# Kernel tuning notes

Hardware: AMD Instinct MI355X
Metric: run time of the kernel (lower is better)

The kernel has to match this reference:

```python
import jax, jax.numpy as jnp
import numpy as np

NOISE_STD = 0.1

def setup_inputs() -> dict:
    key = jax.random.key(0)
    k1, k2, k3, k4 = jax.random.split(key, 4)
    B, S, D, E, NS = 4, 4096, 2048, 64, 10
    x = jax.random.normal(k1, (B, S, D), dtype=jnp.float32)
    W = jax.random.normal(k2, (E, D), dtype=jnp.float32) * (1.0 / np.sqrt(D))
    scale_condition = jax.random.normal(k3, (NS, 1, 1), dtype=jnp.float32)
    noise = jax.random.normal(k4, (B, S, E), dtype=jnp.float32)
    return {"x": x, "W": W, "scale_condition": scale_condition, "noise": noise, "scale_idx": 3}

def reference(x, W, scale_condition, noise, scale_idx):
    TOP_K = 2
    E = W.shape[0]
    # scale modulation: scale_condition[scale_idx] has shape [1,1], broadcasts over [B,S,D]
    scale_factor = scale_condition[scale_idx]
    router_input = x * (1.0 + scale_factor * 0.1)
    # small GEMM: [B,S,D] x [D,E] -> [B,S,E]
    router_logits = jnp.einsum('bsd,ed->bse', router_input, W)
    router_logits = router_logits + noise * NOISE_STD
    routing_probs = jax.nn.softmax(router_logits, axis=-1)
    routing_weights, selected_experts = jax.lax.top_k(routing_probs, TOP_K)
    routing_weights = routing_weights / jnp.sum(routing_weights, axis=-1, keepdims=True)
    # scatter top-k normalized weights into dense [B,S,E] dispatch tensor
    dispatch_tensor = jnp.sum(
        jax.nn.one_hot(selected_experts, E, dtype=routing_weights.dtype)
        * routing_weights[..., None],
        axis=-2,
    )
    return dispatch_tensor, routing_probs, selected_experts
```

## Files before the change

kernel.cpp:

```cpp
#include <hip/hip_runtime.h>
#include <math.h>

#define D        2048
#define E        64
#define NROWS    16384
#define BM       32
#define BK       64
#define NT       256
#define KITERS   (D / BK)

__global__ __launch_bounds__(NT)
void gemm_kernel(const float* __restrict__ x,
                 const float* __restrict__ W,
                 const float* __restrict__ scond,
                 const float* __restrict__ noise,
                 const int* __restrict__ sidx,
                 float* __restrict__ logits_out)
{
    __shared__ float4 xs[BM][17];
    __shared__ float4 ws[BK][16];

    const int tid = threadIdx.x;
    const int rowBase = blockIdx.x * BM;

    const float factor = 1.0f + 0.1f * scond[sidx[0]];

    const int xk = tid & 15;
    const int xr = tid >> 4;
    const int we = tid & 63;
    const int wk = tid >> 6;

    const int eg = tid & 15;
    const int rg = tid >> 4;
    const int e0 = eg << 2;

    float acc[2][4];
#pragma unroll
    for (int i = 0; i < 2; ++i)
#pragma unroll
        for (int j = 0; j < 4; ++j) acc[i][j] = 0.f;

    const float* xg = x + (size_t)rowBase * D;

    float4 xb[2], wb[4];
#pragma unroll
    for (int i = 0; i < 2; ++i)
        xb[i] = *(const float4*)(xg + (xr + 16 * i) * D + (xk << 2));
#pragma unroll
    for (int j = 0; j < 4; ++j)
        wb[j] = *(const float4*)(W + we * D + (wk << 4) + (j << 2));

    for (int t = 0; t < KITERS; ++t) {
#pragma unroll
        for (int i = 0; i < 2; ++i) {
            float4 v = xb[i];
            v.x *= factor; v.y *= factor; v.z *= factor; v.w *= factor;
            xs[xr + 16 * i][xk] = v;
        }
        {
            float* wsf = (float*)ws;
#pragma unroll
            for (int j = 0; j < 4; ++j) {
                const int kk = (wk << 4) + (j << 2);
                wsf[(kk + 0) * E + we] = wb[j].x;
                wsf[(kk + 1) * E + we] = wb[j].y;
                wsf[(kk + 2) * E + we] = wb[j].z;
                wsf[(kk + 3) * E + we] = wb[j].w;
            }
        }
        __syncthreads();

        if (t + 1 < KITERS) {
            const int k0 = (t + 1) * BK;
#pragma unroll
            for (int i = 0; i < 2; ++i)
                xb[i] = *(const float4*)(xg + (xr + 16 * i) * D + k0 + (xk << 2));
#pragma unroll
            for (int j = 0; j < 4; ++j)
                wb[j] = *(const float4*)(W + we * D + k0 + (wk << 4) + (j << 2));
        }

#pragma unroll
        for (int kg = 0; kg < 16; ++kg) {
            float4 xv[2], wv[4];
#pragma unroll
            for (int i = 0; i < 2; ++i) xv[i] = xs[rg + 16 * i][kg];
#pragma unroll
            for (int c = 0; c < 4; ++c) wv[c] = ws[(kg << 2) + c][eg];
#pragma unroll
            for (int i = 0; i < 2; ++i) {
                const float x0 = xv[i].x, x1 = xv[i].y, x2 = xv[i].z, x3 = xv[i].w;
                acc[i][0] += x0 * wv[0].x; acc[i][1] += x0 * wv[0].y;
                acc[i][2] += x0 * wv[0].z; acc[i][3] += x0 * wv[0].w;
                acc[i][0] += x1 * wv[1].x; acc[i][1] += x1 * wv[1].y;
                acc[i][2] += x1 * wv[1].z; acc[i][3] += x1 * wv[1].w;
                acc[i][0] += x2 * wv[2].x; acc[i][1] += x2 * wv[2].y;
                acc[i][2] += x2 * wv[2].z; acc[i][3] += x2 * wv[2].w;
                acc[i][0] += x3 * wv[3].x; acc[i][1] += x3 * wv[3].y;
                acc[i][2] += x3 * wv[3].z; acc[i][3] += x3 * wv[3].w;
            }
        }
        __syncthreads();
    }

#pragma unroll
    for (int i = 0; i < 2; ++i) {
        const int gRow = rowBase + rg + 16 * i;
        const float4 nz = *(const float4*)(noise + (size_t)gRow * E + e0);
        float4 o;
        o.x = acc[i][0] + 0.1f * nz.x;
        o.y = acc[i][1] + 0.1f * nz.y;
        o.z = acc[i][2] + 0.1f * nz.z;
        o.w = acc[i][3] + 0.1f * nz.w;
        *(float4*)(logits_out + (size_t)gRow * E + e0) = o;
    }
}

__global__ __launch_bounds__(256)
void topk_kernel(float* __restrict__ probs,
                 float* __restrict__ dispatch,
                 float* __restrict__ sel)
{
    const int lane = threadIdx.x & 63;
    const int wave = threadIdx.x >> 6;
    const int row  = blockIdx.x * 4 + wave;

    const float v = probs[(size_t)row * E + lane];

    float m = v;
#pragma unroll
    for (int off = 32; off > 0; off >>= 1)
        m = fmaxf(m, __shfl_xor(m, off, 64));
    const float p = expf(v - m);
    float s = p;
#pragma unroll
    for (int off = 32; off > 0; off >>= 1)
        s += __shfl_xor(s, off, 64);
    const float prob = p / s;
    probs[(size_t)row * E + lane] = prob;

    float bv = prob; int bi = lane;
#pragma unroll
    for (int off = 32; off > 0; off >>= 1) {
        const float ov = __shfl_xor(bv, off, 64);
        const int   oi = __shfl_xor(bi, off, 64);
        if (ov > bv || (ov == bv && oi < bi)) { bv = ov; bi = oi; }
    }
    float cv = (lane == bi) ? -INFINITY : prob;
    int ci = lane;
#pragma unroll
    for (int off = 32; off > 0; off >>= 1) {
        const float ov = __shfl_xor(cv, off, 64);
        const int   oi = __shfl_xor(ci, off, 64);
        if (ov > cv || (ov == cv && oi < ci)) { cv = ov; ci = oi; }
    }

    const float sum2 = bv + cv;
    float dval = 0.f;
    if (lane == bi) dval = bv / sum2;
    if (lane == ci) dval = cv / sum2;
    dispatch[(size_t)row * E + lane] = dval;

    if (lane == 0) {
        float2 sv; sv.x = (float)bi; sv.y = (float)ci;
        *(float2*)(sel + (size_t)row * 2) = sv;
    }
}

extern "C" void kernel_launch(void* const* d_in, const int* in_sizes, int n_in,
                              void* d_out, int out_size, void* d_ws, size_t ws_size,
                              hipStream_t stream) {
    const float* x     = (const float*)d_in[0];
    const float* W     = (const float*)d_in[1];
    const float* scond = (const float*)d_in[2];
    const float* noise = (const float*)d_in[3];
    const int*   sidx  = (const int*)d_in[4];

    float* out      = (float*)d_out;
    float* dispatch = out;
    float* probs    = out + (size_t)NROWS * E;
    float* sel      = out + 2 * (size_t)NROWS * E;

    gemm_kernel<<<dim3(NROWS / BM), dim3(NT), 0, stream>>>(
        x, W, scond, noise, sidx, probs);
    topk_kernel<<<dim3(NROWS / 4), dim3(256), 0, stream>>>(
        probs, dispatch, sel);
}
```

Before: 246.1 us.

## Stream x tiles into LDS via direct global-to-LDS loads, read W as uniform loads

```diff
diff --git a/kernel.cpp b/kernel.cpp
--- a/kernel.cpp
+++ b/kernel.cpp
@@ -4,12 +4,11 @@
 #define D        2048
 #define E        64
 #define NROWS    16384
-#define BM       32
 #define BK       64
-#define NT       256
 #define KITERS   (D / BK)
+#define XSTRIDE  68
 
-__global__ __launch_bounds__(NT)
+__global__ __launch_bounds__(512)
 void gemm_kernel(const float* __restrict__ x,
                  const float* __restrict__ W,
                  const float* __restrict__ scond,
@@ -17,103 +16,82 @@
                  const int* __restrict__ sidx,
                  float* __restrict__ logits_out)
 {
-    __shared__ float4 xs[BM][17];
-    __shared__ float4 ws[BK][16];
+    __shared__ float xs[2][64 * XSTRIDE];
 
-    const int tid = threadIdx.x;
-    const int rowBase = blockIdx.x * BM;
+    const int tid  = threadIdx.x;
+    const int lane = tid & 63;
+    const int wv   = tid >> 6;
+    const int rowBase = blockIdx.x * 64;
+
+    const int e0 = __builtin_amdgcn_readfirstlane(wv << 3);
 
     const float factor = 1.0f + 0.1f * scond[sidx[0]];
 
-    const int xk = tid & 15;
-    const int xr = tid >> 4;
-    const int we = tid & 63;
-    const int wk = tid >> 6;
+    float acc[8];
+#pragma unroll
+    for (int j = 0; j < 8; ++j) acc[j] = 0.f;
 
-    const int eg = tid & 15;
-    const int rg = tid >> 4;
-    const int e0 = eg << 2;
-
-    float acc[2][4];
 #pragma unroll
-    for (int i = 0; i < 2; ++i)
-#pragma unroll
-        for (int j = 0; j < 4; ++j) acc[i][j] = 0.f;
-
-    const float* xg = x + (size_t)rowBase * D;
-
-    float4 xb[2], wb[4];
-#pragma unroll
-    for (int i = 0; i < 2; ++i)
-        xb[i] = *(const float4*)(xg + (xr + 16 * i) * D + (xk << 2));
-#pragma unroll
-    for (int j = 0; j < 4; ++j)
-        wb[j] = *(const float4*)(W + we * D + (wk << 4) + (j << 2));
+    for (int rr = 0; rr < 8; ++rr) {
+        const int r = (wv << 3) + rr;
+        const float* src = x + (size_t)(rowBase + r) * D + lane;
+        __builtin_amdgcn_global_load_lds(
+            (const __attribute__((address_space(1))) void*)src,
+            (__attribute__((address_space(3))) void*)&xs[0][r * XSTRIDE],
+            4, 0, 0);
+    }
+    __syncthreads();
 
     for (int t = 0; t < KITERS; ++t) {
+        const int cur = t & 1;
+
+        if (t + 1 < KITERS) {
+            const int nxt = cur ^ 1;
+            const int kOff = (t + 1) * BK;
 #pragma unroll
-        for (int i = 0; i < 2; ++i) {
-            float4 v = xb[i];
-            v.x *= factor; v.y *= factor; v.z *= factor; v.w *= factor;
-            xs[xr + 16 * i][xk] = v;
-        }
-        {
-            float* wsf = (float*)ws;
-#pragma unroll
-            for (int j = 0; j < 4; ++j) {
-                const int kk = (wk << 4) + (j << 2);
-                wsf[(kk + 0) * E + we] = wb[j].x;
-                wsf[(kk + 1) * E + we] = wb[j].y;
-                wsf[(kk + 2) * E + we] = wb[j].z;
-                wsf[(kk + 3) * E + we] = wb[j].w;
+            for (int rr = 0; rr < 8; ++rr) {
+                const int r = (wv << 3) + rr;
+                const float* src = x + (size_t)(rowBase + r) * D + kOff + lane;
+                __builtin_amdgcn_global_load_lds(
+                    (const __attribute__((address_space(1))) void*)src,
+                    (__attribute__((address_space(3))) void*)&xs[nxt][r * XSTRIDE],
+                    4, 0, 0);
             }
         }
-        __syncthreads();
 
-        if (t + 1 < KITERS) {
-            const int k0 = (t + 1) * BK;
-#pragma unroll
-            for (int i = 0; i < 2; ++i)
-                xb[i] = *(const float4*)(xg + (xr + 16 * i) * D + k0 + (xk << 2));
-#pragma unroll
-            for (int j = 0; j < 4; ++j)
-                wb[j] = *(const float4*)(W + we * D + k0 + (wk << 4) + (j << 2));
-        }
-
+        const float4* xrow = (const float4*)&xs[cur][lane * XSTRIDE];
+        const float*  wbaseT = W + (size_t)e0 * D + t * BK;
 #pragma unroll
         for (int kg = 0; kg < 16; ++kg) {
-            float4 xv[2], wv[4];
+            float4 xv = xrow[kg];
+            xv.x *= factor; xv.y *= factor; xv.z *= factor; xv.w *= factor;
+            const float* wb = wbaseT + (kg << 2);
 #pragma unroll
-            for (int i = 0; i < 2; ++i) xv[i] = xs[rg + 16 * i][kg];
-#pragma unroll
-            for (int c = 0; c < 4; ++c) wv[c] = ws[(kg << 2) + c][eg];
-#pragma unroll
-            for (int i = 0; i < 2; ++i) {
-                const float x0 = xv[i].x, x1 = xv[i].y, x2 = xv[i].z, x3 = xv[i].w;
-                acc[i][0] += x0 * wv[0].x; acc[i][1] += x0 * wv[0].y;
-                acc[i][2] += x0 * wv[0].z; acc[i][3] += x0 * wv[0].w;
-                acc[i][0] += x1 * wv[1].x; acc[i][1] += x1 * wv[1].y;
-                acc[i][2] += x1 * wv[1].z; acc[i][3] += x1 * wv[1].w;
-                acc[i][0] += x2 * wv[2].x; acc[i][1] += x2 * wv[2].y;
-                acc[i][2] += x2 * wv[2].z; acc[i][3] += x2 * wv[2].w;
-                acc[i][0] += x3 * wv[3].x; acc[i][1] += x3 * wv[3].y;
-                acc[i][2] += x3 * wv[3].z; acc[i][3] += x3 * wv[3].w;
+            for (int j = 0; j < 8; ++j) {
+                const float4 wq = *(const float4*)(wb + (size_t)j * D);
+                acc[j] += xv.x * wq.x;
+                acc[j] += xv.y * wq.y;
+                acc[j] += xv.z * wq.z;
+                acc[j] += xv.w * wq.w;
             }
         }
         __syncthreads();
     }
 
-#pragma unroll
-    for (int i = 0; i < 2; ++i) {
-        const int gRow = rowBase + rg + 16 * i;
-        const float4 nz = *(const float4*)(noise + (size_t)gRow * E + e0);
-        float4 o;
-        o.x = acc[i][0] + 0.1f * nz.x;
-        o.y = acc[i][1] + 0.1f * nz.y;
-        o.z = acc[i][2] + 0.1f * nz.z;
-        o.w = acc[i][3] + 0.1f * nz.w;
-        *(float4*)(logits_out + (size_t)gRow * E + e0) = o;
-    }
+    const int gRow = rowBase + lane;
+    const float4 n0 = *(const float4*)(noise + (size_t)gRow * E + e0);
+    const float4 n1 = *(const float4*)(noise + (size_t)gRow * E + e0 + 4);
+    float4 o0, o1;
+    o0.x = acc[0] + 0.1f * n0.x;
+    o0.y = acc[1] + 0.1f * n0.y;
+    o0.z = acc[2] + 0.1f * n0.z;
+    o0.w = acc[3] + 0.1f * n0.w;
+    o1.x = acc[4] + 0.1f * n1.x;
+    o1.y = acc[5] + 0.1f * n1.y;
+    o1.z = acc[6] + 0.1f * n1.z;
+    o1.w = acc[7] + 0.1f * n1.w;
+    *(float4*)(logits_out + (size_t)gRow * E + e0)     = o0;
+    *(float4*)(logits_out + (size_t)gRow * E + e0 + 4) = o1;
 }
 
 __global__ __launch_bounds__(256)
@@ -181,7 +159,7 @@
     float* probs    = out + (size_t)NROWS * E;
     float* sel      = out + 2 * (size_t)NROWS * E;
 
-    gemm_kernel<<<dim3(NROWS / BM), dim3(NT), 0, stream>>>(
+    gemm_kernel<<<dim3(NROWS / 64), dim3(512), 0, stream>>>(
         x, W, scond, noise, sidx, probs);
     topk_kernel<<<dim3(NROWS / 4), dim3(256), 0, stream>>>(
         probs, dispatch, sel);
```

After: 444.5 us. 1.81x slower.

## Split-K router GEMM with larger register tiles and fused reduce-softmax-topk

Applied to the files above, without the earlier changes.

```diff
diff --git a/kernel.cpp b/kernel.cpp
--- a/kernel.cpp
+++ b/kernel.cpp
@@ -4,44 +4,193 @@
 #define D        2048
 #define E        64
 #define NROWS    16384
-#define BM       32
-#define BK       64
-#define NT       256
-#define KITERS   (D / BK)
-
-__global__ __launch_bounds__(NT)
-void gemm_kernel(const float* __restrict__ x,
+#define NSLICE   8
+#define KSLICE   (D / NSLICE)
+#define BK       32
+#define TILES    (KSLICE / BK)
+#define BM       128
+#define PARTIAL_BYTES ((size_t)NSLICE * NROWS * E * 4)
+
+__global__ __launch_bounds__(128, 2)
+void gemm_ksplit(const float* __restrict__ x,
                  const float* __restrict__ W,
                  const float* __restrict__ scond,
+                 const int* __restrict__ sidx,
+                 float* __restrict__ partial)
+{
+    __shared__ float4 xsT[8 * 129];
+    __shared__ float  ws [BK * E];
+
+    const int tid   = threadIdx.x;
+    const int slice = blockIdx.x & 7;
+    const int rowBase = (blockIdx.x >> 3) * BM;
+    const int kBase   = slice * KSLICE;
+
+    const float factor = 1.0f + 0.1f * scond[sidx[0]];
+
+    const int sxr = tid >> 3;
+    const int sxc = tid & 7;
+    const int swe = tid & 63;
+    const int swh = tid >> 6;
+
+    const int rg = tid & 15;
+    const int eg = tid >> 4;
+
+    float acc[8][8];
+#pragma unroll
+    for (int i = 0; i < 8; ++i)
+#pragma unroll
+        for (int j = 0; j < 8; ++j) acc[i][j] = 0.f;
+
+    const float* xg = x + (size_t)rowBase * D + kBase;
+    const float* wg = W + (size_t)swe * D + kBase + swh * 16;
+
+    float4 xb[8], wb[4];
+#pragma unroll
+    for (int i = 0; i < 8; ++i)
+        xb[i] = *(const float4*)(xg + (size_t)(sxr + 16 * i) * D + (sxc << 2));
+#pragma unroll
+    for (int j = 0; j < 4; ++j)
+        wb[j] = *(const float4*)(wg + (j << 2));
+
+    for (int t = 0; t < TILES; ++t) {
+#pragma unroll
+        for (int i = 0; i < 8; ++i) {
+            float4 v = xb[i];
+            v.x *= factor; v.y *= factor; v.z *= factor; v.w *= factor;
+            xsT[sxc * 129 + sxr + 16 * i] = v;
+        }
+#pragma unroll
+        for (int j = 0; j < 4; ++j) {
+            const int kk = swh * 16 + (j << 2);
+            ws[(kk + 0) * E + swe] = wb[j].x;
+            ws[(kk + 1) * E + swe] = wb[j].y;
+            ws[(kk + 2) * E + swe] = wb[j].z;
+            ws[(kk + 3) * E + swe] = wb[j].w;
+        }
+        __syncthreads();
+
+        if (t + 1 < TILES) {
+            const int k0 = (t + 1) * BK;
+#pragma unroll
+            for (int i = 0; i < 8; ++i)
+                xb[i] = *(const float4*)(xg + (size_t)(sxr + 16 * i) * D + k0 + (sxc << 2));
+#pragma unroll
+            for (int j = 0; j < 4; ++j)
+                wb[j] = *(const float4*)(wg + k0 + (j << 2));
+        }
+
+        const float4* ws4 = (const float4*)ws;
+#pragma unroll
+        for (int kg = 0; kg < 8; ++kg) {
+            float4 xv[8];
+#pragma unroll
+            for (int i = 0; i < 8; ++i)
+                xv[i] = xsT[kg * 129 + rg + 16 * i];
+#pragma unroll
+            for (int k = 0; k < 4; ++k) {
+                const float4 wa = ws4[((kg << 2) + k) * 16 + (eg << 1)];
+                const float4 wbq = ws4[((kg << 2) + k) * 16 + (eg << 1) + 1];
+#pragma unroll
+                for (int i = 0; i < 8; ++i) {
+                    const float xk = ((const float*)&xv[i])[k];
+                    acc[i][0] += xk * wa.x;  acc[i][1] += xk * wa.y;
+                    acc[i][2] += xk * wa.z;  acc[i][3] += xk * wa.w;
+                    acc[i][4] += xk * wbq.x; acc[i][5] += xk * wbq.y;
+                    acc[i][6] += xk * wbq.z; acc[i][7] += xk * wbq.w;
+                }
+            }
+        }
+        __syncthreads();
+    }
+
+    float* pbase = partial + (size_t)slice * NROWS * E;
+#pragma unroll
+    for (int i = 0; i < 8; ++i) {
+        const int row = rowBase + rg + 16 * i;
+        float4 a0, a1;
+        a0.x = acc[i][0]; a0.y = acc[i][1]; a0.z = acc[i][2]; a0.w = acc[i][3];
+        a1.x = acc[i][4]; a1.y = acc[i][5]; a1.z = acc[i][6]; a1.w = acc[i][7];
+        *(float4*)(pbase + (size_t)row * E + (eg << 3))     = a0;
+        *(float4*)(pbase + (size_t)row * E + (eg << 3) + 4) = a1;
+    }
+}
+
+__global__ __launch_bounds__(256)
+void reduce_topk(const float* __restrict__ partial,
                  const float* __restrict__ noise,
-                 const int* __restrict__ sidx,
-                 float* __restrict__ logits_out)
+                 float* __restrict__ dispatch,
+                 float* __restrict__ probs,
+                 float* __restrict__ sel)
 {
-    __shared__ float4 xs[BM][17];
-    __shared__ float4 ws[BK][16];
-
+    const int lane = threadIdx.x & 63;
+    const int wave = threadIdx.x >> 6;
+    const int row  = blockIdx.x * 4 + wave;
+
+    float v = 0.f;
+#pragma unroll
+    for (int s = 0; s < NSLICE; ++s)
+        v += partial[(size_t)s * NROWS * E + (size_t)row * E + lane];
+    v += 0.1f * noise[(size_t)row * E + lane];
+
+    float m = v;
+#pragma unroll
+    for (int off = 32; off > 0; off >>= 1)
+        m = fmaxf(m, __shfl_xor(m, off, 64));
+    const float p = expf(v - m);
+    float s = p;
+#pragma unroll
+    for (int off = 32; off > 0; off >>= 1)
+        s += __shfl_xor(s, off, 64);
+    const float prob = p / s;
+    probs[(size_t)row * E + lane] = prob;
+
+    float bv = prob; int bi = lane;
+#pragma unroll
+    for (int off = 32; off > 0; off >>= 1) {
+        const float ov = __shfl_xor(bv, off, 64);
+        const int   oi = __shfl_xor(bi, off, 64);
+        if (ov > bv || (ov == bv && oi < bi)) { bv = ov; bi = oi; }
+    }
+    float cv = (lane == bi) ? -INFINITY : prob;
+    int ci = lane;
+#pragma unroll
+    for (int off = 32; off > 0; off >>= 1) {
+        const float ov = __shfl_xor(cv, off, 64);
+        const int   oi = __shfl_xor(ci, off, 64);
+        if (ov > cv || (ov == cv && oi < ci)) { cv = ov; ci = oi; }
+    }
+
+    const float sum2 = bv + cv;
+    float dval = 0.f;
+    if (lane == bi) dval = bv / sum2;
+    if (lane == ci) dval = cv / sum2;
+    dispatch[(size_t)row * E + lane] = dval;
+
+    if (lane == 0) {
+        float2 sv; sv.x = (float)bi; sv.y = (float)ci;
+        *(float2*)(sel + (size_t)row * 2) = sv;
+    }
+}
+
+__global__ __launch_bounds__(256)
+void gemm_r2(const float* __restrict__ x, const float* __restrict__ W,
+             const float* __restrict__ scond, const float* __restrict__ noise,
+             const int* __restrict__ sidx, float* __restrict__ logits_out)
+{
+    __shared__ float4 xs[32][17];
+    __shared__ float4 wsh[64][16];
     const int tid = threadIdx.x;
-    const int rowBase = blockIdx.x * BM;
-
+    const int rowBase = blockIdx.x * 32;
     const float factor = 1.0f + 0.1f * scond[sidx[0]];
-
-    const int xk = tid & 15;
-    const int xr = tid >> 4;
-    const int we = tid & 63;
-    const int wk = tid >> 6;
-
-    const int eg = tid & 15;
-    const int rg = tid >> 4;
-    const int e0 = eg << 2;
-
+    const int xk = tid & 15, xr = tid >> 4, we = tid & 63, wk = tid >> 6;
+    const int eg = tid & 15, rg = tid >> 4, e0 = eg << 2;
     float acc[2][4];
 #pragma unroll
     for (int i = 0; i < 2; ++i)
 #pragma unroll
         for (int j = 0; j < 4; ++j) acc[i][j] = 0.f;
-
     const float* xg = x + (size_t)rowBase * D;
-
     float4 xb[2], wb[4];
 #pragma unroll
     for (int i = 0; i < 2; ++i)
@@ -49,29 +198,25 @@
 #pragma unroll
     for (int j = 0; j < 4; ++j)
         wb[j] = *(const float4*)(W + we * D + (wk << 4) + (j << 2));
-
-    for (int t = 0; t < KITERS; ++t) {
+    for (int t = 0; t < 32; ++t) {
 #pragma unroll
         for (int i = 0; i < 2; ++i) {
             float4 v = xb[i];
             v.x *= factor; v.y *= factor; v.z *= factor; v.w *= factor;
             xs[xr + 16 * i][xk] = v;
         }
-        {
-            float* wsf = (float*)ws;
-#pragma unroll
-            for (int j = 0; j < 4; ++j) {
-                const int kk = (wk << 4) + (j << 2);
-                wsf[(kk + 0) * E + we] = wb[j].x;
-                wsf[(kk + 1) * E + we] = wb[j].y;
-                wsf[(kk + 2) * E + we] = wb[j].z;
-                wsf[(kk + 3) * E + we] = wb[j].w;
-            }
+        float* wsf = (float*)wsh;
+#pragma unroll
+        for (int j = 0; j < 4; ++j) {
+            const int kk = (wk << 4) + (j << 2);
+            wsf[(kk + 0) * E + we] = wb[j].x;
+            wsf[(kk + 1) * E + we] = wb[j].y;
+            wsf[(kk + 2) * E + we] = wb[j].z;
+            wsf[(kk + 3) * E + we] = wb[j].w;
         }
         __syncthreads();
-
-        if (t + 1 < KITERS) {
-            const int k0 = (t + 1) * BK;
+        if (t + 1 < 32) {
+            const int k0 = (t + 1) * 64;
 #pragma unroll
             for (int i = 0; i < 2; ++i)
                 xb[i] = *(const float4*)(xg + (xr + 16 * i) * D + k0 + (xk << 2));
@@ -79,14 +224,13 @@
             for (int j = 0; j < 4; ++j)
                 wb[j] = *(const float4*)(W + we * D + k0 + (wk << 4) + (j << 2));
         }
-
 #pragma unroll
         for (int kg = 0; kg < 16; ++kg) {
             float4 xv[2], wv[4];
 #pragma unroll
             for (int i = 0; i < 2; ++i) xv[i] = xs[rg + 16 * i][kg];
 #pragma unroll
-            for (int c = 0; c < 4; ++c) wv[c] = ws[(kg << 2) + c][eg];
+            for (int c = 0; c < 4; ++c) wv[c] = wsh[(kg << 2) + c][eg];
 #pragma unroll
             for (int i = 0; i < 2; ++i) {
                 const float x0 = xv[i].x, x1 = xv[i].y, x2 = xv[i].z, x3 = xv[i].w;
@@ -102,31 +246,25 @@
         }
         __syncthreads();
     }
-
 #pragma unroll
     for (int i = 0; i < 2; ++i) {
         const int gRow = rowBase + rg + 16 * i;
         const float4 nz = *(const float4*)(noise + (size_t)gRow * E + e0);
         float4 o;
-        o.x = acc[i][0] + 0.1f * nz.x;
-        o.y = acc[i][1] + 0.1f * nz.y;
-        o.z = acc[i][2] + 0.1f * nz.z;
-        o.w = acc[i][3] + 0.1f * nz.w;
+        o.x = acc[i][0] + 0.1f * nz.x; o.y = acc[i][1] + 0.1f * nz.y;
+        o.z = acc[i][2] + 0.1f * nz.z; o.w = acc[i][3] + 0.1f * nz.w;
         *(float4*)(logits_out + (size_t)gRow * E + e0) = o;
     }
 }
 
 __global__ __launch_bounds__(256)
-void topk_kernel(float* __restrict__ probs,
-                 float* __restrict__ dispatch,
-                 float* __restrict__ sel)
+void topk_r2(float* __restrict__ probs, float* __restrict__ dispatch,
+             float* __restrict__ sel)
 {
     const int lane = threadIdx.x & 63;
     const int wave = threadIdx.x >> 6;
     const int row  = blockIdx.x * 4 + wave;
-
     const float v = probs[(size_t)row * E + lane];
-
     float m = v;
 #pragma unroll
     for (int off = 32; off > 0; off >>= 1)
@@ -138,7 +276,6 @@
         s += __shfl_xor(s, off, 64);
     const float prob = p / s;
     probs[(size_t)row * E + lane] = prob;
-
     float bv = prob; int bi = lane;
 #pragma unroll
     for (int off = 32; off > 0; off >>= 1) {
@@ -154,13 +291,11 @@
         const int   oi = __shfl_xor(ci, off, 64);
         if (ov > cv || (ov == cv && oi < ci)) { cv = ov; ci = oi; }
     }
-
     const float sum2 = bv + cv;
     float dval = 0.f;
     if (lane == bi) dval = bv / sum2;
     if (lane == ci) dval = cv / sum2;
     dispatch[(size_t)row * E + lane] = dval;
-
     if (lane == 0) {
         float2 sv; sv.x = (float)bi; sv.y = (float)ci;
         *(float2*)(sel + (size_t)row * 2) = sv;
@@ -181,8 +316,16 @@
     float* probs    = out + (size_t)NROWS * E;
     float* sel      = out + 2 * (size_t)NROWS * E;
 
-    gemm_kernel<<<dim3(NROWS / BM), dim3(NT), 0, stream>>>(
-        x, W, scond, noise, sidx, probs);
-    topk_kernel<<<dim3(NROWS / 4), dim3(256), 0, stream>>>(
-        probs, dispatch, sel);
-}
+    if (ws_size >= PARTIAL_BYTES) {
+        float* partial = (float*)d_ws;
+        gemm_ksplit<<<dim3((NROWS / BM) * NSLICE), dim3(128), 0, stream>>>(
+            x, W, scond, sidx, partial);
+        reduce_topk<<<dim3(NROWS / 4), dim3(256), 0, stream>>>(
+            partial, noise, dispatch, probs, sel);
+    } else {
+        gemm_r2<<<dim3(NROWS / 32), dim3(256), 0, stream>>>(
+            x, W, scond, noise, sidx, probs);
+        topk_r2<<<dim3(NROWS / 4), dim3(256), 0, stream>>>(
+            probs, dispatch, sel);
+    }
+}
```

New measurement: 339.7 us. 1.38x slower.
